# Kernel tuning notes

Measured on AMD Instinct MI355X. Metric: run time of the kernel, lower is better.

The kernel has to match this reference:

```python
import jax, jax.numpy as jnp
import numpy as np

N = 25000   # nodes
E = 600000  # edges (multiple of 48)
IN, H, OUT = 128, 256, 128
SLOPE = 0.01  # LeakyReLU default negative_slope


def _lin(x, w, b):
    return x @ w.T + b


def _leaky(v):
    return jnp.where(v > 0, v, SLOPE * v)


def _sage(x, src, dst, lw, lb, rw):
    # PyG SAGEConv (aggr='mean', root_weight=True, normalize=False):
    # out = lin_l(mean_{j in N(i)} x_j) + lin_r(x_i)
    agg = jax.ops.segment_sum(x[src], dst, num_segments=N)
    deg = jax.ops.segment_sum(jnp.ones((src.shape[0],), x.dtype), dst, num_segments=N)
    mean = agg / jnp.maximum(deg, 1.0)[:, None]
    return mean @ lw.T + lb + x @ rw.T


def setup_inputs() -> dict:
    key = jax.random.key(0)
    ks = jax.random.split(key, 32)

    def w(k, o, i):
        return jax.random.normal(k, (o, i), jnp.float32) * (1.0 / np.sqrt(i))

    def b(k, o):
        return jax.random.normal(k, (o,), jnp.float32) * 0.01

    inp = {
        'x': jax.random.normal(ks[0], (N, IN), jnp.float32),
        'edge_index': jax.random.randint(ks[1], (2, E), 0, N, dtype=jnp.int32),
        'edge_attr': jax.random.normal(ks[2], (E, 1), jnp.float32),
        'batch': jnp.zeros((N,), jnp.int32),
        'prelin_w': w(ks[3], H, IN), 'prelin_b': b(ks[4], H),
        'conv1_lw': w(ks[5], H, H), 'conv1_lb': b(ks[6], H), 'conv1_rw': w(ks[7], H, H),
        'conv2_lw': w(ks[8], H, H), 'conv2_lb': b(ks[9], H), 'conv2_rw': w(ks[10], H, H),
        'conv3_lw': w(ks[11], OUT, H), 'conv3_lb': b(ks[12], OUT), 'conv3_rw': w(ks[13], OUT, H),
        'hh1_w': w(ks[14], H, H), 'hh1_b': b(ks[15], H),
        'hh2_w': w(ks[16], H, H), 'hh2_b': b(ks[17], H),
        'oo_w': w(ks[18], OUT, OUT), 'oo_b': b(ks[19], OUT),
        'lin96_w': w(ks[20], 1, 192), 'lin96_b': b(ks[21], 1),
        'lin32_w': w(ks[22], 1, 64), 'lin32_b': b(ks[23], 1),
    }
    return inp


def reference(x, edge_index, edge_attr, batch,
              prelin_w, prelin_b,
              conv1_lw, conv1_lb, conv1_rw,
              conv2_lw, conv2_lb, conv2_rw,
              conv3_lw, conv3_lb, conv3_rw,
              hh1_w, hh1_b, hh2_w, hh2_b,
              oo_w, oo_b, lin96_w, lin96_b, lin32_w, lin32_b):
    src, dst = edge_index[0], edge_index[1]
    h = jax.nn.relu(_lin(x, prelin_w, prelin_b))
    h = jax.nn.relu(_sage(h, src, dst, conv1_lw, conv1_lb, conv1_rw))
    h = _leaky(_lin(h, hh1_w, hh1_b))
    h = jax.nn.relu(_sage(h, src, dst, conv2_lw, conv2_lb, conv2_rw))
    h = _leaky(_lin(h, hh2_w, hh2_b))
    h = jax.nn.relu(_sage(h, src, dst, conv3_lw, conv3_lb, conv3_rw))
    h = _leaky(_lin(h, oo_w, oo_b))  # [N, 128]

    xl = h[src]  # edge_left  = edge_index[0]
    xr = h[dst]  # edge_right = edge_index[1]
    f96 = jnp.concatenate([xl[:, :96], xr[:, :96]], axis=1)  # [E, 192]
    f32 = jnp.concatenate([xl[:, 96:], xr[:, 96:]], axis=1)  # [E, 64]
    f96 = jax.nn.relu(_lin(f96, lin96_w, lin96_b))  # [E, 1]
    f32 = jax.nn.relu(_lin(f32, lin32_w, lin32_b))  # [E, 1]
    edge_out = f96 * edge_attr + f32                # [E, 1]
    edge_out = edge_out.reshape(-1, 48).mean(axis=1).reshape(-1, 1)  # [E/48, 1]
    return edge_out
```

## Files before the change

kernel.cpp:

```cpp
#include <hip/hip_runtime.h>
#include <hip/hip_bf16.h>

#define N_NODES 25000
#define N_EDGES 600000
#define ACT_NONE 0
#define ACT_RELU 1
#define ACT_LEAKY 2

typedef __bf16 bf16x8 __attribute__((ext_vector_type(8)));
typedef float f32x4 __attribute__((ext_vector_type(4)));
typedef unsigned short u16x8 __attribute__((ext_vector_type(8)));
typedef unsigned short u16x4 __attribute__((ext_vector_type(4)));
typedef short s16x4 __attribute__((ext_vector_type(4)));

__device__ __forceinline__ unsigned short f2bf(float x) {
    union { float f; unsigned int u; } v; v.f = x;
    unsigned int r = (v.u + 0x7fffu + ((v.u >> 16) & 1u)) >> 16;
    return (unsigned short)r;
}
__device__ __forceinline__ float bf2f(unsigned short b) {
    union { float f; unsigned int u; } v; v.u = ((unsigned int)b) << 16;
    return v.f;
}

__global__ __launch_bounds__(256) void hist_kernel(const int* __restrict__ dst,
                                                   int* __restrict__ deg, int E) {
    int e = blockIdx.x * 256 + threadIdx.x;
    if (e < E) atomicAdd(&deg[dst[e]], 1);
}

__global__ __launch_bounds__(1024) void scan_kernel(const int* __restrict__ deg,
                                                    int* __restrict__ off,
                                                    int* __restrict__ cursor, int n) {
    __shared__ int wsum[16];
    int t = threadIdx.x, w = t >> 6, l = t & 63;
    int carry = 0;
    for (int base = 0; base < n; base += 1024) {
        int v = (base + t < n) ? deg[base + t] : 0;
        int x = v;
        #pragma unroll
        for (int d = 1; d < 64; d <<= 1) {
            int y = __shfl_up(x, d);
            if (l >= d) x += y;
        }
        if (l == 63) wsum[w] = x;
        __syncthreads();
        if (w == 0 && l < 16) {
            int s = wsum[l];
            #pragma unroll
            for (int d = 1; d < 16; d <<= 1) {
                int y = __shfl_up(s, d);
                if (l >= d) s += y;
            }
            wsum[l] = s;
        }
        __syncthreads();
        int woff = (w > 0) ? wsum[w - 1] : 0;
        int excl = x + woff - v;
        if (base + t < n) {
            off[base + t] = carry + excl;
            cursor[base + t] = carry + excl;
        }
        int total = wsum[15];
        __syncthreads();
        carry += total;
    }
    if (t == 0) off[n] = carry;
}

__global__ __launch_bounds__(256) void scatter_kernel(const int* __restrict__ src,
                                                      const int* __restrict__ dst,
                                                      int* __restrict__ cursor,
                                                      int* __restrict__ csr_src, int E) {
    int e = blockIdx.x * 256 + threadIdx.x;
    if (e < E) {
        int d = dst[e];
        int pos = atomicAdd(&cursor[d], 1);
        csr_src[pos] = src[e];
    }
}

__global__ __launch_bounds__(256) void convert_kernel(const float* __restrict__ src,
                                                      unsigned short* __restrict__ hi,
                                                      unsigned short* __restrict__ lo, int n) {
    int i = blockIdx.x * 256 + threadIdx.x;
    if (i < n) {
        float x = src[i];
        unsigned short h = f2bf(x);
        hi[i] = h;
        lo[i] = f2bf(x - bf2f(h));
    }
}

struct CvtBatch {
    const float* src[10];
    unsigned short* hi[10];
    unsigned short* lo[10];
    int count[10];
};
__global__ __launch_bounds__(256) void convert_batch_kernel(CvtBatch b) {
    int seg = blockIdx.y;
    int n = b.count[seg];
    int i = blockIdx.x * 256 + threadIdx.x;
    if (i >= n) return;
    float x = b.src[seg][i];
    unsigned short h = f2bf(x);
    b.hi[seg][i] = h;
    b.lo[seg][i] = f2bf(x - bf2f(h));
}

__global__ __launch_bounds__(256) void sage_mean_kernel(const short* __restrict__ qt,
                                                        const float* __restrict__ qs4,
                                                        const int* __restrict__ off,
                                                        const int* __restrict__ csr_src,
                                                        unsigned short* __restrict__ mh,
                                                        unsigned short* __restrict__ ml) {
    int node = blockIdx.x * 4 + (threadIdx.x >> 6);
    if (node >= N_NODES) return;
    int lane = threadIdx.x & 63;
    int qidx = lane >> 4;
    int s0 = off[node], s1 = off[node + 1];
    f32x4 acc0 = {0.f, 0.f, 0.f, 0.f}, acc1 = {0.f, 0.f, 0.f, 0.f};
    f32x4 acc2 = {0.f, 0.f, 0.f, 0.f}, acc3 = {0.f, 0.f, 0.f, 0.f};
    long loff = (long)lane * 4;
    int e = s0;
    for (; e + 4 <= s1; e += 4) {
        int iA = csr_src[e], iB = csr_src[e + 1], iC = csr_src[e + 2], iD = csr_src[e + 3];
        s16x4 qa = *(const s16x4*)&qt[(long)iA * 256 + loff];
        s16x4 qb = *(const s16x4*)&qt[(long)iB * 256 + loff];
        s16x4 qc = *(const s16x4*)&qt[(long)iC * 256 + loff];
        s16x4 qd = *(const s16x4*)&qt[(long)iD * 256 + loff];
        float sa = qs4[(long)iA * 4 + qidx], sb = qs4[(long)iB * 4 + qidx];
        float sc = qs4[(long)iC * 4 + qidx], sd = qs4[(long)iD * 4 + qidx];
        #pragma unroll
        for (int j = 0; j < 4; ++j) {
            acc0[j] += sa * (float)qa[j];
            acc1[j] += sb * (float)qb[j];
            acc2[j] += sc * (float)qc[j];
            acc3[j] += sd * (float)qd[j];
        }
    }
    for (; e < s1; ++e) {
        int iA = csr_src[e];
        s16x4 qa = *(const s16x4*)&qt[(long)iA * 256 + loff];
        float sa = qs4[(long)iA * 4 + qidx];
        #pragma unroll
        for (int j = 0; j < 4; ++j) acc0[j] += sa * (float)qa[j];
    }
    float inv = 1.0f / fmaxf((float)(s1 - s0), 1.0f);
    f32x4 m = ((acc0 + acc1) + (acc2 + acc3)) * inv;
    u16x4 hb, lb;
    #pragma unroll
    for (int j = 0; j < 4; ++j) {
        unsigned short hv = f2bf(m[j]);
        hb[j] = hv;
        lb[j] = f2bf(m[j] - bf2f(hv));
    }
    long base = (long)node * 256 + loff;
    *(u16x4*)&mh[base] = hb;
    *(u16x4*)&ml[base] = lb;
}

__global__ __launch_bounds__(256, 2) void gemm_mfma_kernel(
    const unsigned short* __restrict__ A1h, const unsigned short* __restrict__ A1l,
    const unsigned short* __restrict__ W1h, const unsigned short* __restrict__ W1l,
    const unsigned short* __restrict__ A2h, const unsigned short* __restrict__ A2l,
    const unsigned short* __restrict__ W2h, const unsigned short* __restrict__ W2l,
    const float* __restrict__ bias,
    float* __restrict__ Cf, unsigned short* __restrict__ Ch, unsigned short* __restrict__ Cl,
    short* __restrict__ Cq, float* __restrict__ Cqs,
    int M, int K, int O, int act)
{
    __shared__ unsigned short sAh[128][64];
    __shared__ unsigned short sAl[128][64];
    __shared__ unsigned short sWh[128][64];
    __shared__ unsigned short sWl[128][64];

    int tid = threadIdx.x;
    int row0 = blockIdx.x * 128;
    int col0 = blockIdx.y * 128;
    int wid = tid >> 6, lane = tid & 63;
    int wm = (wid >> 1) * 64, wo = (wid & 1) * 64;
    int fr = lane & 15, qk = lane >> 4;
    int rr = lane >> 3, qq = lane & 7;
    int shalf = (qq >> 2) * 32, scq = qq & 3;

    const int nt1 = K >> 6;
    const int nt  = (A2h != nullptr) ? (nt1 << 1) : nt1;

    f32x4 acc[4][4] = {};

    for (int t = 0; t < nt; ++t) {
        const unsigned short *Ah, *Al, *Wh, *Wl;
        int k0;
        if (t < nt1) { Ah = A1h; Al = A1l; Wh = W1h; Wl = W1l; k0 = t << 6; }
        else         { Ah = A2h; Al = A2l; Wh = W2h; Wl = W2l; k0 = (t - nt1) << 6; }

        #pragma unroll
        for (int i = 0; i < 4; ++i) {
            int rb = wid * 32 + i * 8;
            int r  = rb + rr;
            int gs = shalf + ((scq + (r >> 1)) & 3) * 8;
            long ar = (long)(row0 + r); if (ar > M - 1) ar = M - 1;
            long wr = (long)(col0 + r);
            __builtin_amdgcn_global_load_lds(
                (const __attribute__((address_space(1))) unsigned int*)(Ah + ar * K + k0 + gs),
                (__attribute__((address_space(3))) unsigned int*)&sAh[rb][0], 16, 0, 0);
            __builtin_amdgcn_global_load_lds(
                (const __attribute__((address_space(1))) unsigned int*)(Al + ar * K + k0 + gs),
                (__attribute__((address_space(3))) unsigned int*)&sAl[rb][0], 16, 0, 0);
            __builtin_amdgcn_global_load_lds(
                (const __attribute__((address_space(1))) unsigned int*)(Wh + wr * K + k0 + gs),
                (__attribute__((address_space(3))) unsigned int*)&sWh[rb][0], 16, 0, 0);
            __builtin_amdgcn_global_load_lds(
                (const __attribute__((address_space(1))) unsigned int*)(Wl + wr * K + k0 + gs),
                (__attribute__((address_space(3))) unsigned int*)&sWl[rb][0], 16, 0, 0);
        }
        __syncthreads();

        #pragma unroll
        for (int kk = 0; kk < 2; ++kk) {
            bf16x8 ah[4], al[4], bh[4], bl[4];
            #pragma unroll
            for (int i = 0; i < 4; ++i) {
                int rowA = wm + i * 16 + fr;
                int offA = rowA * 64 + kk * 32 + 8 * ((qk - (rowA >> 1)) & 3);
                ah[i] = *(const bf16x8*)(&sAh[0][0] + offA);
                al[i] = *(const bf16x8*)(&sAl[0][0] + offA);
                int rowB = wo + i * 16 + fr;
                int offB = rowB * 64 + kk * 32 + 8 * ((qk - (rowB >> 1)) & 3);
                bh[i] = *(const bf16x8*)(&sWh[0][0] + offB);
                bl[i] = *(const bf16x8*)(&sWl[0][0] + offB);
            }
            #pragma unroll
            for (int i = 0; i < 4; ++i) {
                #pragma unroll
                for (int j = 0; j < 4; ++j) {
                    acc[i][j] = __builtin_amdgcn_mfma_f32_16x16x32_bf16(ah[i], bh[j], acc[i][j], 0, 0, 0);
                    acc[i][j] = __builtin_amdgcn_mfma_f32_16x16x32_bf16(ah[i], bl[j], acc[i][j], 0, 0, 0);
                    acc[i][j] = __builtin_amdgcn_mfma_f32_16x16x32_bf16(al[i], bh[j], acc[i][j], 0, 0, 0);
                }
            }
        }
        __syncthreads();
    }

    int rgrp = (lane >> 4) * 4;
    int cl_ = lane & 15;
    int quarter = (col0 + wo) >> 6;
    #pragma unroll
    for (int i = 0; i < 4; ++i) {
        float bv[4];
        #pragma unroll
        for (int j = 0; j < 4; ++j) bv[j] = bias[col0 + wo + j * 16 + cl_];
        #pragma unroll
        for (int r = 0; r < 4; ++r) {
            int grow = row0 + wm + i * 16 + rgrp + r;
            float vv[4];
            float m = 0.0f;
            #pragma unroll
            for (int j = 0; j < 4; ++j) {
                float v = acc[i][j][r] + bv[j];
                if (act == ACT_RELU)       v = fmaxf(v, 0.0f);
                else if (act == ACT_LEAKY) v = (v > 0.0f) ? v : 0.01f * v;
                vv[j] = v;
                m = fmaxf(m, fabsf(v));
            }
            float qinv = 0.0f;
            if (Cq) {
                #pragma unroll
                for (int d = 1; d < 16; d <<= 1) m = fmaxf(m, __shfl_xor(m, d));
                qinv = (m > 0.0f) ? 32767.0f / m : 0.0f;
            }
            bool ok = grow < M;
            #pragma unroll
            for (int j = 0; j < 4; ++j) {
                int gcol = col0 + wo + j * 16 + cl_;
                long idx = (long)grow * O + gcol;
                if (ok) {
                    float v = vv[j];
                    if (Cf) Cf[idx] = v;
                    if (Ch) {
                        unsigned short hbits = f2bf(v);
                        Ch[idx] = hbits;
                        Cl[idx] = f2bf(v - bf2f(hbits));
                    }
                    if (Cq) Cq[idx] = (short)(int)rintf(v * qinv);
                }
            }
            if (Cq && ok && cl_ == 0)
                Cqs[(long)grow * 4 + quarter] = (m > 0.0f) ? m / 32767.0f : 0.0f;
        }
    }
}

__global__ __launch_bounds__(256) void node_dots_kernel(const float* __restrict__ h,
                                                        const float* __restrict__ w96,
                                                        const float* __restrict__ w32,
                                                        float* __restrict__ nodeDot) {
    int node = blockIdx.x * 4 + (threadIdx.x >> 6);
    if (node >= N_NODES) return;
    int lane = threadIdx.x & 63;
    const float* row = h + (long)node * 128;
    float h0 = row[lane];
    float h1 = row[64 + lane];
    float pL96 = h0 * w96[lane];
    float pR96 = h0 * w96[96 + lane];
    float pL32 = 0.0f, pR32 = 0.0f;
    if (lane < 32) {
        pL96 += h1 * w96[64 + lane];
        pR96 += h1 * w96[160 + lane];
    } else {
        int k = lane - 32;
        pL32 = h1 * w32[k];
        pR32 = h1 * w32[32 + k];
    }
    #pragma unroll
    for (int m = 32; m > 0; m >>= 1) {
        pL96 += __shfl_xor(pL96, m);
        pR96 += __shfl_xor(pR96, m);
        pL32 += __shfl_xor(pL32, m);
        pR32 += __shfl_xor(pR32, m);
    }
    if (lane == 0) {
        f32x4 v = {pL96, pR96, pL32, pR32};
        *(f32x4*)&nodeDot[(long)node * 4] = v;
    }
}

__global__ __launch_bounds__(256) void edge_group_kernel(const float* __restrict__ nodeDot,
                                                         const int* __restrict__ src,
                                                         const int* __restrict__ dst,
                                                         const float* __restrict__ eattr,
                                                         const float* __restrict__ b96,
                                                         const float* __restrict__ b32,
                                                         float* __restrict__ out, int G) {
    int g = blockIdx.x * 256 + threadIdx.x;
    if (g >= G) return;
    float bb96 = b96[0], bb32 = b32[0];
    int base = g * 48;
    float s = 0.0f;
    #pragma unroll 4
    for (int k = 0; k < 48; ++k) {
        int e = base + k;
        f32x4 a = *(const f32x4*)&nodeDot[(long)src[e] * 4];
        f32x4 b = *(const f32x4*)&nodeDot[(long)dst[e] * 4];
        float f96  = fmaxf(a[0] + b[1] + bb96, 0.0f);
        float f32v = fmaxf(a[2] + b[3] + bb32, 0.0f);
        s += f96 * eattr[e] + f32v;
    }
    out[g] = s * (1.0f / 48.0f);
}

extern "C" void kernel_launch(void* const* d_in, const int* in_sizes, int n_in,
                              void* d_out, int out_size, void* d_ws, size_t ws_size,
                              hipStream_t stream) {
    const float* x         = (const float*)d_in[0];
    const int*   edge_idx  = (const int*)d_in[1];
    const float* edge_attr = (const float*)d_in[2];
    const float* prelin_w  = (const float*)d_in[4];
    const float* prelin_b  = (const float*)d_in[5];
    const float* conv1_lw  = (const float*)d_in[6];
    const float* conv1_lb  = (const float*)d_in[7];
    const float* conv1_rw  = (const float*)d_in[8];
    const float* conv2_lw  = (const float*)d_in[9];
    const float* conv2_lb  = (const float*)d_in[10];
    const float* conv2_rw  = (const float*)d_in[11];
    const float* conv3_lw  = (const float*)d_in[12];
    const float* conv3_lb  = (const float*)d_in[13];
    const float* conv3_rw  = (const float*)d_in[14];
    const float* hh1_w     = (const float*)d_in[15];
    const float* hh1_b     = (const float*)d_in[16];
    const float* hh2_w     = (const float*)d_in[17];
    const float* hh2_b     = (const float*)d_in[18];
    const float* oo_w      = (const float*)d_in[19];
    const float* oo_b      = (const float*)d_in[20];
    const float* lin96_w   = (const float*)d_in[21];
    const float* lin96_b   = (const float*)d_in[22];
    const float* lin32_w   = (const float*)d_in[23];
    const float* lin32_b   = (const float*)d_in[24];

    const int* src = edge_idx;
    const int* dst = edge_idx + N_EDGES;

    char* wsp = (char*)d_ws;
    size_t used = 0;
    auto alloc = [&](size_t bytes) -> char* {
        char* r = wsp;
        size_t pad = (bytes + 255) & ~(size_t)255;
        wsp += pad; used += pad;
        return r;
    };
    float* bufF = (float*)alloc((size_t)N_NODES * 256 * 4);
    unsigned short* P0h = (unsigned short*)alloc((size_t)N_NODES * 256 * 2);
    unsigned short* P0l = (unsigned short*)alloc((size_t)N_NODES * 256 * 2);
    unsigned short* P1h = (unsigned short*)alloc((size_t)N_NODES * 256 * 2);
    unsigned short* P1l = (unsigned short*)alloc((size_t)N_NODES * 256 * 2);
    unsigned short* P2h = (unsigned short*)alloc((size_t)N_NODES * 256 * 2);
    unsigned short* P2l = (unsigned short*)alloc((size_t)N_NODES * 256 * 2);
    short* qtab    = (short*)alloc((size_t)N_NODES * 256 * 2);
    float* qsc4    = (float*)alloc((size_t)N_NODES * 4 * 4);
    float* nodeDot = (float*)alloc((size_t)N_NODES * 4 * 4);
    int* deg       = (int*)alloc((size_t)N_NODES * 4);
    int* off       = (int*)alloc((size_t)(N_NODES + 1) * 4);
    int* cursor    = (int*)alloc((size_t)N_NODES * 4);
    int* csr_src   = (int*)alloc((size_t)N_EDGES * 4);

    struct WP { unsigned short *h, *l; };
    auto wpair = [&](int n) -> WP {
        WP w; w.h = (unsigned short*)alloc((size_t)n * 2);
        w.l = (unsigned short*)alloc((size_t)n * 2); return w;
    };
    WP w_pre = wpair(256 * 128);
    WP w_c1l = wpair(256 * 256), w_c1r = wpair(256 * 256);
    WP w_c2l = wpair(256 * 256), w_c2r = wpair(256 * 256);
    WP w_c3l = wpair(128 * 256), w_c3r = wpair(128 * 256);
    WP w_h1  = wpair(256 * 256), w_h2 = wpair(256 * 256);
    WP w_oo  = wpair(128 * 128);

    if (used > ws_size) return;

    const int EB = (N_EDGES + 255) / 256;
    const int MB = (N_NODES + 127) / 128;
    const int NB4 = (N_NODES + 3) / 4;

    (void)hipMemsetAsync(deg, 0, N_NODES * sizeof(int), stream);
    hist_kernel<<<EB, 256, 0, stream>>>(dst, deg, N_EDGES);
    scan_kernel<<<1, 1024, 0, stream>>>(deg, off, cursor, N_NODES);
    scatter_kernel<<<EB, 256, 0, stream>>>(src, dst, cursor, csr_src, N_EDGES);

    convert_kernel<<<((N_NODES * 128) + 255) / 256, 256, 0, stream>>>(x, P0h, P0l, N_NODES * 128);
    CvtBatch cb;
    const float* wsrc[10] = {prelin_w, conv1_lw, conv1_rw, conv2_lw, conv2_rw,
                             conv3_lw, conv3_rw, hh1_w, hh2_w, oo_w};
    WP wdst[10] = {w_pre, w_c1l, w_c1r, w_c2l, w_c2r, w_c3l, w_c3r, w_h1, w_h2, w_oo};
    int wcnt[10] = {256 * 128, 256 * 256, 256 * 256, 256 * 256, 256 * 256,
                    128 * 256, 128 * 256, 256 * 256, 256 * 256, 128 * 128};
    for (int i = 0; i < 10; ++i) {
        cb.src[i] = wsrc[i]; cb.hi[i] = wdst[i].h; cb.lo[i] = wdst[i].l; cb.count[i] = wcnt[i];
    }
    convert_batch_kernel<<<dim3((65536 + 255) / 256, 10), 256, 0, stream>>>(cb);

    gemm_mfma_kernel<<<dim3(MB, 2), 256, 0, stream>>>(
        P0h, P0l, w_pre.h, w_pre.l, nullptr, nullptr, nullptr, nullptr,
        prelin_b, nullptr, P1h, P1l, qtab, qsc4, N_NODES, 128, 256, ACT_RELU);

    sage_mean_kernel<<<NB4, 256, 0, stream>>>(qtab, qsc4, off, csr_src, P2h, P2l);
    gemm_mfma_kernel<<<dim3(MB, 2), 256, 0, stream>>>(
        P2h, P2l, w_c1l.h, w_c1l.l, P1h, P1l, w_c1r.h, w_c1r.l,
        conv1_lb, nullptr, P0h, P0l, nullptr, nullptr, N_NODES, 256, 256, ACT_RELU);
    gemm_mfma_kernel<<<dim3(MB, 2), 256, 0, stream>>>(
        P0h, P0l, w_h1.h, w_h1.l, nullptr, nullptr, nullptr, nullptr,
        hh1_b, nullptr, P1h, P1l, qtab, qsc4, N_NODES, 256, 256, ACT_LEAKY);

    sage_mean_kernel<<<NB4, 256, 0, stream>>>(qtab, qsc4, off, csr_src, P2h, P2l);
    gemm_mfma_kernel<<<dim3(MB, 2), 256, 0, stream>>>(
        P2h, P2l, w_c2l.h, w_c2l.l, P1h, P1l, w_c2r.h, w_c2r.l,
        conv2_lb, nullptr, P0h, P0l, nullptr, nullptr, N_NODES, 256, 256, ACT_RELU);
    gemm_mfma_kernel<<<dim3(MB, 2), 256, 0, stream>>>(
        P0h, P0l, w_h2.h, w_h2.l, nullptr, nullptr, nullptr, nullptr,
        hh2_b, nullptr, P1h, P1l, qtab, qsc4, N_NODES, 256, 256, ACT_LEAKY);

    sage_mean_kernel<<<NB4, 256, 0, stream>>>(qtab, qsc4, off, csr_src, P2h, P2l);
    gemm_mfma_kernel<<<dim3(MB, 1), 256, 0, stream>>>(
        P2h, P2l, w_c3l.h, w_c3l.l, P1h, P1l, w_c3r.h, w_c3r.l,
        conv3_lb, nullptr, P0h, P0l, nullptr, nullptr, N_NODES, 256, 128, ACT_RELU);
    gemm_mfma_kernel<<<dim3(MB, 1), 256, 0, stream>>>(
        P0h, P0l, w_oo.h, w_oo.l, nullptr, nullptr, nullptr, nullptr,
        oo_b, bufF, nullptr, nullptr, nullptr, nullptr, N_NODES, 128, 128, ACT_LEAKY);

    node_dots_kernel<<<NB4, 256, 0, stream>>>(bufF, lin96_w, lin32_w, nodeDot);
    const int G = N_EDGES / 48;
    edge_group_kernel<<<(G + 255) / 256, 256, 0, stream>>>(
        nodeDot, src, dst, edge_attr, lin96_b, lin32_b, (float*)d_out, G);
}
```

Baseline: 441.0 us.

## Double-buffer GEMM LDS tiles with K=32 stages to overlap loads and MFMA

The single K=64 shared-memory tile in the split-bf16 MFMA GEMM becomes two K=32 buffers. The next tile's global_load_lds is issued before computing on the current one, with an explicit vmcnt wait and raw s_barrier. This hides global-to-LDS latency behind MFMA work. In exchange there are twice as many barriers per unit of K and fewer MFMAs between syncs, and the hand-counted vmcnt must stay correct for the number of loads issued.

```diff
diff --git a/kernel.cpp b/kernel.cpp
--- a/kernel.cpp
+++ b/kernel.cpp
@@ -171,10 +171,10 @@
     short* __restrict__ Cq, float* __restrict__ Cqs,
     int M, int K, int O, int act)
 {
-    __shared__ unsigned short sAh[128][64];
-    __shared__ unsigned short sAl[128][64];
-    __shared__ unsigned short sWh[128][64];
-    __shared__ unsigned short sWl[128][64];
+    __shared__ unsigned short sAh[2][128][32];
+    __shared__ unsigned short sAl[2][128][32];
+    __shared__ unsigned short sWh[2][128][32];
+    __shared__ unsigned short sWl[2][128][32];
 
     int tid = threadIdx.x;
     int row0 = blockIdx.x * 128;
@@ -182,67 +182,76 @@
     int wid = tid >> 6, lane = tid & 63;
     int wm = (wid >> 1) * 64, wo = (wid & 1) * 64;
     int fr = lane & 15, qk = lane >> 4;
-    int rr = lane >> 3, qq = lane & 7;
-    int shalf = (qq >> 2) * 32, scq = qq & 3;
-
-    const int nt1 = K >> 6;
+    int rr = lane >> 2, qq = lane & 3;
+
+    const int nt1 = K >> 5;
     const int nt  = (A2h != nullptr) ? (nt1 << 1) : nt1;
 
     f32x4 acc[4][4] = {};
 
-    for (int t = 0; t < nt; ++t) {
+    auto STAGE = [&](int buf, int t) {
         const unsigned short *Ah, *Al, *Wh, *Wl;
         int k0;
-        if (t < nt1) { Ah = A1h; Al = A1l; Wh = W1h; Wl = W1l; k0 = t << 6; }
-        else         { Ah = A2h; Al = A2l; Wh = W2h; Wl = W2l; k0 = (t - nt1) << 6; }
-
-        #pragma unroll
-        for (int i = 0; i < 4; ++i) {
-            int rb = wid * 32 + i * 8;
-            int r  = rb + rr;
-            int gs = shalf + ((scq + (r >> 1)) & 3) * 8;
-            long ar = (long)(row0 + r); if (ar > M - 1) ar = M - 1;
+        if (t < nt1) { Ah = A1h; Al = A1l; Wh = W1h; Wl = W1l; k0 = t << 5; }
+        else         { Ah = A2h; Al = A2l; Wh = W2h; Wl = W2l; k0 = (t - nt1) << 5; }
+        #pragma unroll
+        for (int i = 0; i < 2; ++i) {
+            int rb = wid * 32 + i * 16;
+            int r = rb + rr;
+            int gc = ((qq + (r >> 1)) & 3) * 8;
+            long ar = (long)(row0 + r);
+            if (ar > M - 1) ar = M - 1;
             long wr = (long)(col0 + r);
             __builtin_amdgcn_global_load_lds(
-                (const __attribute__((address_space(1))) unsigned int*)(Ah + ar * K + k0 + gs),
-                (__attribute__((address_space(3))) unsigned int*)&sAh[rb][0], 16, 0, 0);
+                (const __attribute__((address_space(1))) unsigned int*)(Ah + ar * K + k0 + gc),
+                (__attribute__((address_space(3))) unsigned int*)&sAh[buf][rb][0], 16, 0, 0);
             __builtin_amdgcn_global_load_lds(
-                (const __attribute__((address_space(1))) unsigned int*)(Al + ar * K + k0 + gs),
-                (__attribute__((address_space(3))) unsigned int*)&sAl[rb][0], 16, 0, 0);
+                (const __attribute__((address_space(1))) unsigned int*)(Al + ar * K + k0 + gc),
+                (__attribute__((address_space(3))) unsigned int*)&sAl[buf][rb][0], 16, 0, 0);
             __builtin_amdgcn_global_load_lds(
-                (const __attribute__((address_space(1))) unsigned int*)(Wh + wr * K + k0 + gs),
-                (__attribute__((address_space(3))) unsigned int*)&sWh[rb][0], 16, 0, 0);
+                (const __attribute__((address_space(1))) unsigned int*)(Wh + wr * K + k0 + gc),
+                (__attribute__((address_space(3))) unsigned int*)&sWh[buf][rb][0], 16, 0, 0);
             __builtin_amdgcn_global_load_lds(
-                (const __attribute__((address_space(1))) unsigned int*)(Wl + wr * K + k0 + gs),
-                (__attribute__((address_space(3))) unsigned int*)&sWl[rb][0], 16, 0, 0);
-        }
-        __syncthreads();
-
-        #pragma unroll
-        for (int kk = 0; kk < 2; ++kk) {
-            bf16x8 ah[4], al[4], bh[4], bl[4];
+                (const __attribute__((address_space(1))) unsigned int*)(Wl + wr * K + k0 + gc),
+                (__attribute__((address_space(3))) unsigned int*)&sWl[buf][rb][0], 16, 0, 0);
+        }
+    };
+
+    STAGE(0, 0);
+
+    for (int t = 0; t < nt; ++t) {
+        int cur = t & 1;
+        if (t + 1 < nt) {
+            STAGE(cur ^ 1, t + 1);
+            asm volatile("s_waitcnt vmcnt(8)" ::: "memory");
+        } else {
+            asm volatile("s_waitcnt vmcnt(0)" ::: "memory");
+        }
+        __builtin_amdgcn_s_barrier();
+        __builtin_amdgcn_sched_barrier(0);
+
+        bf16x8 ah[4], al[4], bh[4], bl[4];
+        #pragma unroll
+        for (int i = 0; i < 4; ++i) {
+            int rowA = wm + i * 16 + fr;
+            int offA = rowA * 32 + 8 * ((qk - (rowA >> 1)) & 3);
+            ah[i] = *(const bf16x8*)(&sAh[cur][0][0] + offA);
+            al[i] = *(const bf16x8*)(&sAl[cur][0][0] + offA);
+            int rowB = wo + i * 16 + fr;
+            int offB = rowB * 32 + 8 * ((qk - (rowB >> 1)) & 3);
+            bh[i] = *(const bf16x8*)(&sWh[cur][0][0] + offB);
+            bl[i] = *(const bf16x8*)(&sWl[cur][0][0] + offB);
+        }
+        #pragma unroll
+        for (int i = 0; i < 4; ++i) {
             #pragma unroll
-            for (int i = 0; i < 4; ++i) {
-                int rowA = wm + i * 16 + fr;
-                int offA = rowA * 64 + kk * 32 + 8 * ((qk - (rowA >> 1)) & 3);
-                ah[i] = *(const bf16x8*)(&sAh[0][0] + offA);
-                al[i] = *(const bf16x8*)(&sAl[0][0] + offA);
-                int rowB = wo + i * 16 + fr;
-                int offB = rowB * 64 + kk * 32 + 8 * ((qk - (rowB >> 1)) & 3);
-                bh[i] = *(const bf16x8*)(&sWh[0][0] + offB);
-                bl[i] = *(const bf16x8*)(&sWl[0][0] + offB);
+            for (int j = 0; j < 4; ++j) {
+                acc[i][j] = __builtin_amdgcn_mfma_f32_16x16x32_bf16(ah[i], bh[j], acc[i][j], 0, 0, 0);
+                acc[i][j] = __builtin_amdgcn_mfma_f32_16x16x32_bf16(ah[i], bl[j], acc[i][j], 0, 0, 0);
+                acc[i][j] = __builtin_amdgcn_mfma_f32_16x16x32_bf16(al[i], bh[j], acc[i][j], 0, 0, 0);
             }
-            #pragma unroll
-            for (int i = 0; i < 4; ++i) {
-                #pragma unroll
-                for (int j = 0; j < 4; ++j) {
-                    acc[i][j] = __builtin_amdgcn_mfma_f32_16x16x32_bf16(ah[i], bh[j], acc[i][j], 0, 0, 0);
-                    acc[i][j] = __builtin_amdgcn_mfma_f32_16x16x32_bf16(ah[i], bl[j], acc[i][j], 0, 0, 0);
-                    acc[i][j] = __builtin_amdgcn_mfma_f32_16x16x32_bf16(al[i], bh[j], acc[i][j], 0, 0, 0);
-                }
-            }
-        }
-        __syncthreads();
+        }
+        __builtin_amdgcn_s_barrier();
     }
 
     int rgrp = (lane >> 4) * 4;
```

Result: slower. 457.4 us (+3.7%).
